# Kernel optimization log

Measured on AMD Instinct MI355X. Metric: run time of the kernel, lower is better.

The kernel has to match this reference:

```python
import jax, jax.numpy as jnp
import numpy as np

DT = 0.01
HID = 64
IN_DIM = 13  # obs_dim(6) + dynamic state(7)
G_VEC = jnp.array([0.0, 0.0, 9.81], dtype=jnp.float32)
MAG_REF = jnp.array([20.0, 0.0, -40.0], dtype=jnp.float32)


def q_multiply(q1, q2):
    w1, x1, y1, z1 = q1[:, 0], q1[:, 1], q1[:, 2], q1[:, 3]
    w2, x2, y2, z2 = q2[:, 0], q2[:, 1], q2[:, 2], q2[:, 3]
    w = w1 * w2 - x1 * x2 - y1 * y2 - z1 * z2
    x = w1 * x2 + x1 * w2 + y1 * z2 - z1 * y2
    y = w1 * y2 - x1 * z2 + y1 * w2 + z1 * x2
    z = w1 * z2 + x1 * y2 - y1 * x2 + z1 * w2
    return jnp.stack((w, x, y, z), axis=1)


def q_to_rot(q):
    w, x, y, z = q[:, 0], q[:, 1], q[:, 2], q[:, 3]
    r00 = 1 - 2 * (y * y + z * z); r01 = 2 * (x * y - z * w); r02 = 2 * (x * z + y * w)
    r10 = 2 * (x * y + z * w); r11 = 1 - 2 * (x * x + z * z); r12 = 2 * (y * z - x * w)
    r20 = 2 * (x * z - y * w); r21 = 2 * (y * z + x * w); r22 = 1 - 2 * (x * x + y * y)
    row0 = jnp.stack((r00, r01, r02), axis=1)
    row1 = jnp.stack((r10, r11, r12), axis=1)
    row2 = jnp.stack((r20, r21, r22), axis=1)
    return jnp.stack((row0, row1, row2), axis=1)  # [B,3,3]


def rotate_vec(q, v):
    return jnp.einsum('bij,bj->bi', q_to_rot(q), v)


def rotate_vec_inverse(q, v):
    return jnp.einsum('bji,bj->bi', q_to_rot(q), v)  # R^T v


def layer_norm(x, gamma, beta, eps=1e-5):
    mu = jnp.mean(x, axis=-1, keepdims=True)
    var = jnp.mean((x - mu) ** 2, axis=-1, keepdims=True)
    return (x - mu) * jax.lax.rsqrt(var + eps) * gamma + beta


def gru_cell(x, h, w_ih, w_hh, b_ih, b_hh):
    gi = x @ w_ih.T + b_ih  # [B, 3H]
    gh = h @ w_hh.T + b_hh
    i_r, i_z, i_n = jnp.split(gi, 3, axis=-1)
    h_r, h_z, h_n = jnp.split(gh, 3, axis=-1)
    r = jax.nn.sigmoid(i_r + h_r)
    z = jax.nn.sigmoid(i_z + h_z)
    n = jnp.tanh(i_n + r * h_n)
    return (1.0 - z) * n + z * h


def kalmannet_forward(inputs, ln_gamma, ln_beta, w_ih, w_hh, b_ih, b_hh, fc_w, fc_b):
    B, T, _ = inputs.shape
    x0 = jnp.zeros((B, 10), dtype=inputs.dtype).at[:, 6].set(1.0)
    h0 = jnp.zeros((B, HID), dtype=inputs.dtype)
    g_b = jnp.broadcast_to(G_VEC, (B, 3))
    mag_b = jnp.broadcast_to(MAG_REF, (B, 3))

    def step(carry, inp_t):
        x_curr, h_gru = carry
        accel = inp_t[:, 0:3]; gyro = inp_t[:, 3:6]; mag = inp_t[:, 6:9]
        p, v, q = x_curr[:, 0:3], x_curr[:, 3:6], x_curr[:, 6:10]
        # quaternion propagation
        half_ang = gyro * (DT * 0.5)
        dq = jnp.concatenate((jnp.ones((B, 1), inp_t.dtype), half_ang), axis=1)
        dq = dq / jnp.linalg.norm(dq, axis=1, keepdims=True)
        q_pred = q_multiply(q, dq)
        q_pred = q_pred / jnp.linalg.norm(q_pred, axis=1, keepdims=True)
        # strapdown kinematics
        accel_world = rotate_vec(q, accel) - g_b
        v_pred = v + accel_world * DT
        p_pred = p + v * DT + 0.5 * accel_world * (DT * DT)
        x_pred_pv = jnp.concatenate((p_pred, v_pred), axis=1)
        # innovation
        g_body = rotate_vec_inverse(q_pred, g_b)
        mag_body = rotate_vec_inverse(q_pred, mag_b)
        innovation = jnp.concatenate((mag, accel), axis=1) - jnp.concatenate((mag_body, g_body), axis=1)
        # learned Kalman gain
        gru_in = jnp.concatenate((innovation, v_pred, q_pred), axis=1)  # [B,13]
        gru_in = layer_norm(gru_in, ln_gamma, ln_beta)
        h_new = gru_cell(gru_in, h_gru, w_ih, w_hh, b_ih, b_hh)
        K = (h_new @ fc_w.T + fc_b).reshape(B, 6, 6)
        corr = jnp.einsum('bij,bj->bi', K, innovation)
        x_new = jnp.concatenate((x_pred_pv + corr, q_pred), axis=1)
        return (x_new, h_new), x_new

    inputs_t = jnp.swapaxes(inputs, 0, 1)  # [T,B,9]
    _, outs = jax.lax.scan(step, (x0, h0), inputs_t)
    return jnp.swapaxes(outs, 0, 1)  # [B,T,10]


def setup_inputs() -> dict:
    key = jax.random.key(0)
    ks = jax.random.split(key, 4)
    B, T = 4096, 512
    inputs = jax.random.normal(ks[0], (B, T, 9), dtype=jnp.float32)
    w_ih = jax.random.normal(ks[1], (3 * HID, IN_DIM), dtype=jnp.float32) * 0.1
    w_hh = jax.random.normal(ks[2], (3 * HID, HID), dtype=jnp.float32) * 0.1
    fc_w = jax.random.uniform(ks[3], (36, HID), minval=-0.001, maxval=0.001, dtype=jnp.float32)
    return {
        'inputs': inputs,
        'ln_gamma': jnp.ones((IN_DIM,), jnp.float32),
        'ln_beta': jnp.zeros((IN_DIM,), jnp.float32),
        'w_ih': w_ih,
        'w_hh': w_hh,
        'b_ih': jnp.zeros((3 * HID,), jnp.float32),
        'b_hh': jnp.zeros((3 * HID,), jnp.float32),
        'fc_w': fc_w,
        'fc_b': jnp.zeros((36,), jnp.float32),
    }


def reference(inputs, ln_gamma, ln_beta, w_ih, w_hh, b_ih, b_hh, fc_w, fc_b):
    return kalmannet_forward(inputs, ln_gamma, ln_beta, w_ih, w_hh, b_ih, b_hh, fc_w, fc_b)
```

## Files before the change

### kernel.cpp

```cpp
#include <hip/hip_runtime.h>

#define TT 512

typedef _Float16 h2_t  __attribute__((ext_vector_type(2)));
typedef _Float16 f16x4 __attribute__((ext_vector_type(4)));
typedef float    f32x4 __attribute__((ext_vector_type(4)));
typedef float    f32x4u __attribute__((ext_vector_type(4), aligned(4)));
typedef unsigned int u32x2_t __attribute__((ext_vector_type(2)));

__device__ __forceinline__ float frcp(float x){ return __builtin_amdgcn_rcpf(x); }
__device__ __forceinline__ float frsq(float x){ return __builtin_amdgcn_rsqf(x); }
__device__ __forceinline__ float sigm(float x){ return frcp(1.0f + __expf(-x)); }
__device__ __forceinline__ float tanh_fast(float x){
    x = fminf(15.0f, fmaxf(-15.0f, x));
    float e = __expf(2.0f * x);
    return (e - 1.0f) * frcp(e + 1.0f);
}
__device__ __forceinline__ float fdot2(h2_t a, h2_t b, float c){
    return __builtin_amdgcn_fdot2(a, b, c, false);
}
__device__ __forceinline__ h2_t pk16(float a, float b){
    return __builtin_bit_cast(h2_t, __builtin_amdgcn_cvt_pkrtz(a, b));
}
__device__ __forceinline__ f16x4 mk4(float a, float b, float c, float d){
    u32x2_t u;
    u[0] = __builtin_bit_cast(unsigned int, pk16(a, b));
    u[1] = __builtin_bit_cast(unsigned int, pk16(c, d));
    return __builtin_bit_cast(f16x4, u);
}
__device__ __forceinline__ f32x4 mfma16(f16x4 a, f16x4 b, f32x4 c){
    return __builtin_amdgcn_mfma_f32_16x16x16f16(a, b, c, 0, 0, 0);
}

__global__
__attribute__((amdgpu_flat_work_group_size(256, 256), amdgpu_waves_per_eu(1, 1)))
void kalman_kernel(const float* __restrict__ inputs,
                   const float* __restrict__ ln_gamma,
                   const float* __restrict__ ln_beta,
                   const float* __restrict__ w_ih,
                   const float* __restrict__ w_hh,
                   const float* __restrict__ b_ih,
                   const float* __restrict__ b_hh,
                   const float* __restrict__ fc_w,
                   const float* __restrict__ fc_b,
                   float* __restrict__ out)
{
    __shared__ u32x2_t     s_h[4][64];
    __shared__ unsigned int s_Kp[24][16];

    const int tid  = threadIdx.x;
    const int lane = tid & 63;
    const int w    = tid >> 6;
    const int bq   = lane & 15;
    const int g    = lane >> 4;
    const int e    = blockIdx.x * 16 + bq;

    const int mtR = w, mtZ = 4 + w, mtN = 8 + w;

    f16x4 whhR[4], whhZ[4], whhN[4];
#pragma unroll
    for (int kt = 0; kt < 4; ++kt) {
        const float* rR = w_hh + (size_t)(16 * mtR + bq) * 64 + 16 * kt + 4 * g;
        const float* rZ = w_hh + (size_t)(16 * mtZ + bq) * 64 + 16 * kt + 4 * g;
        const float* rN = w_hh + (size_t)(16 * mtN + bq) * 64 + 16 * kt + 4 * g;
        whhR[kt] = mk4(rR[0], rR[1], rR[2], rR[3]);
        whhZ[kt] = mk4(rZ[0], rZ[1], rZ[2], rZ[3]);
        whhN[kt] = mk4(rN[0], rN[1], rN[2], rN[3]);
    }

    f16x4 wihR, wihZ, wihN;
    {
        const float* rR = w_ih + (size_t)(16 * mtR + bq) * 13;
        const float* rZ = w_ih + (size_t)(16 * mtZ + bq) * 13;
        const float* rN = w_ih + (size_t)(16 * mtN + bq) * 13;
        const int k0 = 4 * g;
        const float m1 = (k0 + 1 < 13) ? 1.f : 0.f;
        const float m2 = (k0 + 2 < 13) ? 1.f : 0.f;
        const float m3 = (k0 + 3 < 13) ? 1.f : 0.f;
        wihR = mk4(rR[k0], m1 * rR[k0 + 1], m2 * rR[k0 + 2], m3 * rR[k0 + 3]);
        wihZ = mk4(rZ[k0], m1 * rZ[k0 + 1], m2 * rZ[k0 + 2], m3 * rZ[k0 + 3]);
        wihN = mk4(rN[k0], m1 * rN[k0 + 1], m2 * rN[k0 + 2], m3 * rN[k0 + 3]);
    }

    f16x4 fcA[4];
    {
        const int o = 16 * w + bq;
        const float* rp = fc_w + (size_t)(o < 36 ? o : 0) * 64;
        const float msk = (o < 36) ? 1.f : 0.f;
#pragma unroll
        for (int kt = 0; kt < 4; ++kt) {
            const float* cp = rp + 16 * kt + 4 * g;
            fcA[kt] = mk4(msk * cp[0], msk * cp[1], msk * cp[2], msk * cp[3]);
        }
    }

    f32x4 br, bz, bin, bhn, fcb4;
#pragma unroll
    for (int r = 0; r < 4; ++r) {
        const int oR = 16 * mtR + 4 * g + r;
        const int oZ = 16 * mtZ + 4 * g + r;
        const int oN = 16 * mtN + 4 * g + r;
        br[r]  = b_ih[oR] + b_hh[oR];
        bz[r]  = b_ih[oZ] + b_hh[oZ];
        bin[r] = b_ih[oN];
        bhn[r] = b_hh[oN];
        const int oF = 16 * w + 4 * g + r;
        fcb4[r] = (oF < 36) ? fc_b[oF] : 0.f;
    }

    float gamx[4], betx[4];
#pragma unroll
    for (int j = 0; j < 4; ++j) {
        const int k = 4 * g + j;
        gamx[j] = (k < 13) ? ln_gamma[k] : 0.f;
        betx[j] = (k < 13) ? ln_beta[k]  : 0.f;
    }

    float pos0 = 0, pos1 = 0, pos2 = 0, vel0 = 0, vel1 = 0, vel2 = 0;
    float q0 = 1.0f, q1 = 0, q2 = 0, q3 = 0;
    f32x4 hstate = f32x4{0.f, 0.f, 0.f, 0.f};
    f16x4 hB[4];
#pragma unroll
    for (int i = 0; i < 4; ++i) hB[i] = mk4(0.f, 0.f, 0.f, 0.f);

    const float* ip = inputs + (size_t)e * TT * 9;
    float*       op = out    + (size_t)e * TT * 10;

    float cur[9];
#pragma unroll
    for (int k = 0; k < 9; ++k) cur[k] = ip[k];

    for (int t = 0; t < TT; ++t) {
        f32x4 ar = br, az4 = bz, nhh = bhn;
#pragma unroll
        for (int kt = 0; kt < 4; ++kt) {
            ar  = mfma16(whhR[kt], hB[kt], ar);
            az4 = mfma16(whhZ[kt], hB[kt], az4);
            nhh = mfma16(whhN[kt], hB[kt], nhh);
        }

        const int tn = (t < TT - 1) ? (t + 1) : t;
        float nxt[9];
#pragma unroll
        for (int k = 0; k < 9; ++k) nxt[k] = ip[(size_t)tn * 9 + k];

        const float ax = cur[0], ay = cur[1], az = cur[2];
        const float gx = cur[3], gy = cur[4], gz = cur[5];
        const float mx = cur[6], my = cur[7], mz = cur[8];

        const float hx = gx * 0.005f, hy = gy * 0.005f, hz = gz * 0.005f;
        const float dn = frsq(1.0f + hx * hx + hy * hy + hz * hz);
        const float dw = dn, dx = hx * dn, dy = hy * dn, dz = hz * dn;
        float qpw = q0 * dw - q1 * dx - q2 * dy - q3 * dz;
        float qpx = q0 * dx + q1 * dw + q2 * dz - q3 * dy;
        float qpy = q0 * dy - q1 * dz + q2 * dw + q3 * dx;
        float qpz = q0 * dz + q1 * dy - q2 * dx + q3 * dw;
        const float pn = frsq(qpw * qpw + qpx * qpx + qpy * qpy + qpz * qpz);
        qpw *= pn; qpx *= pn; qpy *= pn; qpz *= pn;

        const float r00 = 1.0f - 2.0f * (q2 * q2 + q3 * q3);
        const float r01 = 2.0f * (q1 * q2 - q3 * q0);
        const float r02 = 2.0f * (q1 * q3 + q2 * q0);
        const float r10 = 2.0f * (q1 * q2 + q3 * q0);
        const float r11 = 1.0f - 2.0f * (q1 * q1 + q3 * q3);
        const float r12 = 2.0f * (q2 * q3 - q1 * q0);
        const float r20 = 2.0f * (q1 * q3 - q2 * q0);
        const float r21 = 2.0f * (q2 * q3 + q1 * q0);
        const float r22 = 1.0f - 2.0f * (q1 * q1 + q2 * q2);
        const float awx = r00 * ax + r01 * ay + r02 * az;
        const float awy = r10 * ax + r11 * ay + r12 * az;
        const float awz = r20 * ax + r21 * ay + r22 * az - 9.81f;

        const float vpx = vel0 + awx * 0.01f;
        const float vpy = vel1 + awy * 0.01f;
        const float vpz = vel2 + awz * 0.01f;
        const float ppx = pos0 + vel0 * 0.01f + awx * 5e-5f;
        const float ppy = pos1 + vel1 * 0.01f + awy * 5e-5f;
        const float ppz = pos2 + vel2 * 0.01f + awz * 5e-5f;

        const float s00 = 1.0f - 2.0f * (qpy * qpy + qpz * qpz);
        const float s01 = 2.0f * (qpx * qpy - qpz * qpw);
        const float s02 = 2.0f * (qpx * qpz + qpy * qpw);
        const float s20 = 2.0f * (qpx * qpz - qpy * qpw);
        const float s21 = 2.0f * (qpy * qpz + qpx * qpw);
        const float s22 = 1.0f - 2.0f * (qpx * qpx + qpy * qpy);
        const float gbx = 9.81f * s20, gby = 9.81f * s21, gbz = 9.81f * s22;
        const float mbx = 20.0f * s00 - 40.0f * s20;
        const float mby = 20.0f * s01 - 40.0f * s21;
        const float mbz = 20.0f * s02 - 40.0f * s22;

        float inn[6];
        inn[0] = mx - mbx; inn[1] = my - mby; inn[2] = mz - mbz;
        inn[3] = ax - gbx; inn[4] = ay - gby; inn[5] = az - gbz;

        float gin[13];
        gin[0] = inn[0]; gin[1] = inn[1]; gin[2] = inn[2];
        gin[3] = inn[3]; gin[4] = inn[4]; gin[5] = inn[5];
        gin[6] = vpx; gin[7] = vpy; gin[8] = vpz;
        gin[9] = qpw; gin[10] = qpx; gin[11] = qpy; gin[12] = qpz;

        float mu = 0.0f;
#pragma unroll
        for (int k = 0; k < 13; ++k) mu += gin[k];
        mu *= (1.0f / 13.0f);
        float var = 0.0f;
#pragma unroll
        for (int k = 0; k < 13; ++k) { const float d = gin[k] - mu; var += d * d; }
        var *= (1.0f / 13.0f);
        const float sc = frsq(var + 1e-5f);

        const float xs0 = g == 0 ? gin[0] : g == 1 ? gin[4] : g == 2 ? gin[8]  : gin[12];
        const float xs1 = g == 0 ? gin[1] : g == 1 ? gin[5] : g == 2 ? gin[9]  : 0.f;
        const float xs2 = g == 0 ? gin[2] : g == 1 ? gin[6] : g == 2 ? gin[10] : 0.f;
        const float xs3 = g == 0 ? gin[3] : g == 1 ? gin[7] : g == 2 ? gin[11] : 0.f;
        const f16x4 xB = mk4((xs0 - mu) * sc * gamx[0] + betx[0],
                             (xs1 - mu) * sc * gamx[1] + betx[1],
                             (xs2 - mu) * sc * gamx[2] + betx[2],
                             (xs3 - mu) * sc * gamx[3] + betx[3]);

        ar  = mfma16(wihR, xB, ar);
        az4 = mfma16(wihZ, xB, az4);
        const f32x4 nin = mfma16(wihN, xB, bin);

        f32x4 hv = hstate;
#pragma unroll
        for (int r = 0; r < 4; ++r) {
            const float rr = sigm(ar[r]);
            const float zz = sigm(az4[r]);
            const float nn = tanh_fast(nin[r] + rr * nhh[r]);
            hv[r] = fmaf(zz, hv[r] - nn, nn);
        }
        hstate = hv;
        const f16x4 hOwn = mk4(hv[0], hv[1], hv[2], hv[3]);

        s_h[w][lane] = __builtin_bit_cast(u32x2_t, hOwn);
        __syncthreads();
#pragma unroll
        for (int kt = 0; kt < 4; ++kt)
            hB[kt] = __builtin_bit_cast(f16x4, s_h[kt][lane]);

        if (w < 3) {
            f32x4 a = mfma16(fcA[0], hB[0], fcb4);
#pragma unroll
            for (int kt = 1; kt < 4; ++kt) a = mfma16(fcA[kt], hB[kt], a);
            s_Kp[8 * w + 2 * g][bq]     = __builtin_bit_cast(unsigned int, pk16(a[0], a[1]));
            s_Kp[8 * w + 2 * g + 1][bq] = __builtin_bit_cast(unsigned int, pk16(a[2], a[3]));
        }
        __syncthreads();

        h2_t K2[18];
#pragma unroll
        for (int rp = 0; rp < 18; ++rp)
            K2[rp] = __builtin_bit_cast(h2_t, s_Kp[rp][bq]);

        const h2_t inn2_0 = pk16(inn[0], inn[1]);
        const h2_t inn2_1 = pk16(inn[2], inn[3]);
        const h2_t inn2_2 = pk16(inn[4], inn[5]);
        float c[6];
#pragma unroll
        for (int i = 0; i < 6; ++i)
            c[i] = fdot2(K2[3 * i + 0], inn2_0,
                   fdot2(K2[3 * i + 1], inn2_1,
                   fdot2(K2[3 * i + 2], inn2_2, 0.f)));

        pos0 = ppx + c[0]; pos1 = ppy + c[1]; pos2 = ppz + c[2];
        vel0 = vpx + c[3]; vel1 = vpy + c[4]; vel2 = vpz + c[5];
        q0 = qpw; q1 = qpx; q2 = qpy; q3 = qpz;

        if (w == 0) {
            float* o0 = op + (size_t)t * 10;
            if (g == 0) {
                *(f32x4u*)(o0) = f32x4u{pos0, pos1, pos2, vel0};
            } else if (g == 1) {
                *(f32x4u*)(o0 + 4) = f32x4u{vel1, vel2, q0, q1};
            } else if (g == 2) {
                o0[8] = q2; o0[9] = q3;
            }
        }

#pragma unroll
        for (int k = 0; k < 9; ++k) cur[k] = nxt[k];
    }
}

extern "C" void kernel_launch(void* const* d_in, const int* in_sizes, int n_in,
                              void* d_out, int out_size, void* d_ws, size_t ws_size,
                              hipStream_t stream) {
    const float* inputs   = (const float*)d_in[0];
    const float* ln_gamma = (const float*)d_in[1];
    const float* ln_beta  = (const float*)d_in[2];
    const float* w_ih     = (const float*)d_in[3];
    const float* w_hh     = (const float*)d_in[4];
    const float* b_ih     = (const float*)d_in[5];
    const float* b_hh     = (const float*)d_in[6];
    const float* fc_w     = (const float*)d_in[7];
    const float* fc_b     = (const float*)d_in[8];
    float* out = (float*)d_out;

    const int B = in_sizes[0] / (TT * 9);
    kalman_kernel<<<dim3(B / 16), dim3(256), 0, stream>>>(
        inputs, ln_gamma, ln_beta, w_ih, w_hh, b_ih, b_hh, fc_w, fc_b, out);
}
```

Baseline: 700.9 us.

## Software-pipeline recurrence: precompute next-step quaternion/innovation work between barriers

Splits each timestep into a HEAD part that depends only on the quaternion and inputs (quaternion propagation, rotation, innovations, partial layer-norm sums) and an ASTEP part needing the Kalman-corrected position and velocity. HEAD for step t+1 now runs while the FC gain MFMA for step t executes, before the barrier, so it leaves the serial critical path. Layer-norm statistics are rebuilt from precomputed partial sums and variance is computed as E[x^2]-mu^2. Inputs are prefetched two steps ahead with vector loads. The single-pass variance can be less accurate, and the restructured loop makes register pressure and control flow more complex.

New measurement: 786.1 us. 1.12x slower.

```diff
diff --git a/kernel.cpp b/kernel.cpp
--- a/kernel.cpp
+++ b/kernel.cpp
@@ -116,8 +116,13 @@
         betx[j] = (k < 13) ? ln_beta[k]  : 0.f;
     }
 
-    float pos0 = 0, pos1 = 0, pos2 = 0, vel0 = 0, vel1 = 0, vel2 = 0;
-    float q0 = 1.0f, q1 = 0, q2 = 0, q3 = 0;
+    float q0 = 1.0f, q1 = 0.f, q2 = 0.f, q3 = 0.f;
+    float qpn0, qpn1, qpn2, qpn3;
+    float aw0, aw1, aw2;
+    float innc0, innc1, innc2, innc3, innc4, innc5;
+    float innx0, innx1, innx2, innx3, innx4, innx5;
+    float S1h, S2h;
+    float vpx, vpy, vpz, ppx, ppy, ppz;
     f32x4 hstate = f32x4{0.f, 0.f, 0.f, 0.f};
     f16x4 hB[4];
 #pragma unroll
@@ -126,37 +131,23 @@
     const float* ip = inputs + (size_t)e * TT * 9;
     float*       op = out    + (size_t)e * TT * 10;
 
-    float cur[9];
+    float cur[9], nxt[9];
 #pragma unroll
     for (int k = 0; k < 9; ++k) cur[k] = ip[k];
 
-    for (int t = 0; t < TT; ++t) {
-        f32x4 ar = br, az4 = bz, nhh = bhn;
-#pragma unroll
-        for (int kt = 0; kt < 4; ++kt) {
-            ar  = mfma16(whhR[kt], hB[kt], ar);
-            az4 = mfma16(whhZ[kt], hB[kt], az4);
-            nhh = mfma16(whhN[kt], hB[kt], nhh);
-        }
-
-        const int tn = (t < TT - 1) ? (t + 1) : t;
-        float nxt[9];
-#pragma unroll
-        for (int k = 0; k < 9; ++k) nxt[k] = ip[(size_t)tn * 9 + k];
-
+    auto HEAD = [&]() {
         const float ax = cur[0], ay = cur[1], az = cur[2];
         const float gx = cur[3], gy = cur[4], gz = cur[5];
         const float mx = cur[6], my = cur[7], mz = cur[8];
-
         const float hx = gx * 0.005f, hy = gy * 0.005f, hz = gz * 0.005f;
         const float dn = frsq(1.0f + hx * hx + hy * hy + hz * hz);
         const float dw = dn, dx = hx * dn, dy = hy * dn, dz = hz * dn;
-        float qpw = q0 * dw - q1 * dx - q2 * dy - q3 * dz;
-        float qpx = q0 * dx + q1 * dw + q2 * dz - q3 * dy;
-        float qpy = q0 * dy - q1 * dz + q2 * dw + q3 * dx;
-        float qpz = q0 * dz + q1 * dy - q2 * dx + q3 * dw;
-        const float pn = frsq(qpw * qpw + qpx * qpx + qpy * qpy + qpz * qpz);
-        qpw *= pn; qpx *= pn; qpy *= pn; qpz *= pn;
+        const float a0 = q0 * dw - q1 * dx - q2 * dy - q3 * dz;
+        const float a1 = q0 * dx + q1 * dw + q2 * dz - q3 * dy;
+        const float a2 = q0 * dy - q1 * dz + q2 * dw + q3 * dx;
+        const float a3 = q0 * dz + q1 * dy - q2 * dx + q3 * dw;
+        const float pn = frsq(a0 * a0 + a1 * a1 + a2 * a2 + a3 * a3);
+        qpn0 = a0 * pn; qpn1 = a1 * pn; qpn2 = a2 * pn; qpn3 = a3 * pn;
 
         const float r00 = 1.0f - 2.0f * (q2 * q2 + q3 * q3);
         const float r01 = 2.0f * (q1 * q2 - q3 * q0);
@@ -167,56 +158,65 @@
         const float r20 = 2.0f * (q1 * q3 - q2 * q0);
         const float r21 = 2.0f * (q2 * q3 + q1 * q0);
         const float r22 = 1.0f - 2.0f * (q1 * q1 + q2 * q2);
-        const float awx = r00 * ax + r01 * ay + r02 * az;
-        const float awy = r10 * ax + r11 * ay + r12 * az;
-        const float awz = r20 * ax + r21 * ay + r22 * az - 9.81f;
-
-        const float vpx = vel0 + awx * 0.01f;
-        const float vpy = vel1 + awy * 0.01f;
-        const float vpz = vel2 + awz * 0.01f;
-        const float ppx = pos0 + vel0 * 0.01f + awx * 5e-5f;
-        const float ppy = pos1 + vel1 * 0.01f + awy * 5e-5f;
-        const float ppz = pos2 + vel2 * 0.01f + awz * 5e-5f;
-
-        const float s00 = 1.0f - 2.0f * (qpy * qpy + qpz * qpz);
-        const float s01 = 2.0f * (qpx * qpy - qpz * qpw);
-        const float s02 = 2.0f * (qpx * qpz + qpy * qpw);
-        const float s20 = 2.0f * (qpx * qpz - qpy * qpw);
-        const float s21 = 2.0f * (qpy * qpz + qpx * qpw);
-        const float s22 = 1.0f - 2.0f * (qpx * qpx + qpy * qpy);
-        const float gbx = 9.81f * s20, gby = 9.81f * s21, gbz = 9.81f * s22;
-        const float mbx = 20.0f * s00 - 40.0f * s20;
-        const float mby = 20.0f * s01 - 40.0f * s21;
-        const float mbz = 20.0f * s02 - 40.0f * s22;
-
-        float inn[6];
-        inn[0] = mx - mbx; inn[1] = my - mby; inn[2] = mz - mbz;
-        inn[3] = ax - gbx; inn[4] = ay - gby; inn[5] = az - gbz;
-
-        float gin[13];
-        gin[0] = inn[0]; gin[1] = inn[1]; gin[2] = inn[2];
-        gin[3] = inn[3]; gin[4] = inn[4]; gin[5] = inn[5];
-        gin[6] = vpx; gin[7] = vpy; gin[8] = vpz;
-        gin[9] = qpw; gin[10] = qpx; gin[11] = qpy; gin[12] = qpz;
-
-        float mu = 0.0f;
-#pragma unroll
-        for (int k = 0; k < 13; ++k) mu += gin[k];
-        mu *= (1.0f / 13.0f);
-        float var = 0.0f;
-#pragma unroll
-        for (int k = 0; k < 13; ++k) { const float d = gin[k] - mu; var += d * d; }
-        var *= (1.0f / 13.0f);
+        aw0 = r00 * ax + r01 * ay + r02 * az;
+        aw1 = r10 * ax + r11 * ay + r12 * az;
+        aw2 = r20 * ax + r21 * ay + r22 * az - 9.81f;
+
+        const float s00 = 1.0f - 2.0f * (qpn2 * qpn2 + qpn3 * qpn3);
+        const float s01 = 2.0f * (qpn1 * qpn2 - qpn3 * qpn0);
+        const float s02 = 2.0f * (qpn1 * qpn3 + qpn2 * qpn0);
+        const float s20 = 2.0f * (qpn1 * qpn3 - qpn2 * qpn0);
+        const float s21 = 2.0f * (qpn2 * qpn3 + qpn1 * qpn0);
+        const float s22 = 1.0f - 2.0f * (qpn1 * qpn1 + qpn2 * qpn2);
+        innx0 = mx - (20.0f * s00 - 40.0f * s20);
+        innx1 = my - (20.0f * s01 - 40.0f * s21);
+        innx2 = mz - (20.0f * s02 - 40.0f * s22);
+        innx3 = ax - 9.81f * s20;
+        innx4 = ay - 9.81f * s21;
+        innx5 = az - 9.81f * s22;
+
+        S1h = ((innx0 + innx1) + (innx2 + innx3)) + ((innx4 + innx5) +
+              (qpn0 + qpn1)) + (qpn2 + qpn3);
+        float s2 = innx0 * innx0;
+        s2 = fmaf(innx1, innx1, s2); s2 = fmaf(innx2, innx2, s2);
+        s2 = fmaf(innx3, innx3, s2); s2 = fmaf(innx4, innx4, s2);
+        s2 = fmaf(innx5, innx5, s2); s2 = fmaf(qpn0, qpn0, s2);
+        s2 = fmaf(qpn1, qpn1, s2);   s2 = fmaf(qpn2, qpn2, s2);
+        s2 = fmaf(qpn3, qpn3, s2);
+        S2h = s2;
+    };
+
+    auto ASTEP = [&](float pn0, float pn1, float pn2,
+                     float vn0, float vn1, float vn2) {
+        f32x4 ar = br, az4 = bz, nhh = bhn;
+#pragma unroll
+        for (int kt = 0; kt < 4; ++kt) {
+            ar  = mfma16(whhR[kt], hB[kt], ar);
+            az4 = mfma16(whhZ[kt], hB[kt], az4);
+            nhh = mfma16(whhN[kt], hB[kt], nhh);
+        }
+
+        vpx = fmaf(aw0, 0.01f, vn0);
+        vpy = fmaf(aw1, 0.01f, vn1);
+        vpz = fmaf(aw2, 0.01f, vn2);
+        ppx = fmaf(vn0, 0.01f, fmaf(aw0, 5e-5f, pn0));
+        ppy = fmaf(vn1, 0.01f, fmaf(aw1, 5e-5f, pn1));
+        ppz = fmaf(vn2, 0.01f, fmaf(aw2, 5e-5f, pn2));
+
+        const float mu = (S1h + ((vpx + vpy) + vpz)) * (1.0f / 13.0f);
+        float s2 = S2h;
+        s2 = fmaf(vpx, vpx, s2); s2 = fmaf(vpy, vpy, s2); s2 = fmaf(vpz, vpz, s2);
+        const float var = fmaf(-mu, mu, s2 * (1.0f / 13.0f));
         const float sc = frsq(var + 1e-5f);
 
-        const float xs0 = g == 0 ? gin[0] : g == 1 ? gin[4] : g == 2 ? gin[8]  : gin[12];
-        const float xs1 = g == 0 ? gin[1] : g == 1 ? gin[5] : g == 2 ? gin[9]  : 0.f;
-        const float xs2 = g == 0 ? gin[2] : g == 1 ? gin[6] : g == 2 ? gin[10] : 0.f;
-        const float xs3 = g == 0 ? gin[3] : g == 1 ? gin[7] : g == 2 ? gin[11] : 0.f;
-        const f16x4 xB = mk4((xs0 - mu) * sc * gamx[0] + betx[0],
-                             (xs1 - mu) * sc * gamx[1] + betx[1],
-                             (xs2 - mu) * sc * gamx[2] + betx[2],
-                             (xs3 - mu) * sc * gamx[3] + betx[3]);
+        const float c0 = g == 0 ? innx0 : g == 1 ? innx4 : g == 2 ? vpz  : qpn3;
+        const float c1 = g == 0 ? innx1 : g == 1 ? innx5 : g == 2 ? qpn0 : 0.f;
+        const float c2 = g == 0 ? innx2 : g == 1 ? vpx   : g == 2 ? qpn1 : 0.f;
+        const float c3 = g == 0 ? innx3 : g == 1 ? vpy   : g == 2 ? qpn2 : 0.f;
+        const f16x4 xB = mk4((c0 - mu) * sc * gamx[0] + betx[0],
+                             (c1 - mu) * sc * gamx[1] + betx[1],
+                             (c2 - mu) * sc * gamx[2] + betx[2],
+                             (c3 - mu) * sc * gamx[3] + betx[3]);
 
         ar  = mfma16(wihR, xB, ar);
         az4 = mfma16(wihZ, xB, az4);
@@ -232,12 +232,33 @@
         }
         hstate = hv;
         const f16x4 hOwn = mk4(hv[0], hv[1], hv[2], hv[3]);
-
         s_h[w][lane] = __builtin_bit_cast(u32x2_t, hOwn);
-        __syncthreads();
+
+        innc0 = innx0; innc1 = innx1; innc2 = innx2;
+        innc3 = innx3; innc4 = innx4; innc5 = innx5;
+        q0 = qpn0; q1 = qpn1; q2 = qpn2; q3 = qpn3;
+    };
+
+    HEAD();
+    ASTEP(0.f, 0.f, 0.f, 0.f, 0.f, 0.f);
+#pragma unroll
+    for (int k = 0; k < 9; ++k) cur[k] = ip[9 + k];
+    __syncthreads();
+
+    for (int t = 0; t < TT; ++t) {
 #pragma unroll
         for (int kt = 0; kt < 4; ++kt)
             hB[kt] = __builtin_bit_cast(f16x4, s_h[kt][lane]);
+
+        {
+            const int tf = (t + 2 < TT) ? (t + 2) : (TT - 1);
+            const float* np = ip + (size_t)tf * 9;
+            const f32x4u v0 = *(const f32x4u*)np;
+            const f32x4u v1 = *(const f32x4u*)(np + 4);
+            nxt[0] = v0[0]; nxt[1] = v0[1]; nxt[2] = v0[2]; nxt[3] = v0[3];
+            nxt[4] = v1[0]; nxt[5] = v1[1]; nxt[6] = v1[2]; nxt[7] = v1[3];
+            nxt[8] = np[8];
+        }
 
         if (w < 3) {
             f32x4 a = mfma16(fcA[0], hB[0], fcb4);
@@ -246,6 +267,8 @@
             s_Kp[8 * w + 2 * g][bq]     = __builtin_bit_cast(unsigned int, pk16(a[0], a[1]));
             s_Kp[8 * w + 2 * g + 1][bq] = __builtin_bit_cast(unsigned int, pk16(a[2], a[3]));
         }
+
+        if (t < TT - 1) HEAD();
         __syncthreads();
 
         h2_t K2[18];
@@ -253,33 +276,36 @@
         for (int rp = 0; rp < 18; ++rp)
             K2[rp] = __builtin_bit_cast(h2_t, s_Kp[rp][bq]);
 
-        const h2_t inn2_0 = pk16(inn[0], inn[1]);
-        const h2_t inn2_1 = pk16(inn[2], inn[3]);
-        const h2_t inn2_2 = pk16(inn[4], inn[5]);
+        const h2_t in0 = pk16(innc0, innc1);
+        const h2_t in1 = pk16(innc2, innc3);
+        const h2_t in2 = pk16(innc4, innc5);
         float c[6];
 #pragma unroll
         for (int i = 0; i < 6; ++i)
-            c[i] = fdot2(K2[3 * i + 0], inn2_0,
-                   fdot2(K2[3 * i + 1], inn2_1,
-                   fdot2(K2[3 * i + 2], inn2_2, 0.f)));
-
-        pos0 = ppx + c[0]; pos1 = ppy + c[1]; pos2 = ppz + c[2];
-        vel0 = vpx + c[3]; vel1 = vpy + c[4]; vel2 = vpz + c[5];
-        q0 = qpw; q1 = qpx; q2 = qpy; q3 = qpz;
+            c[i] = fdot2(K2[3 * i + 0], in0,
+                   fdot2(K2[3 * i + 1], in1,
+                   fdot2(K2[3 * i + 2], in2, 0.f)));
+
+        const float pn0 = ppx + c[0], pn1 = ppy + c[1], pn2 = ppz + c[2];
+        const float vn0 = vpx + c[3], vn1 = vpy + c[4], vn2 = vpz + c[5];
 
         if (w == 0) {
             float* o0 = op + (size_t)t * 10;
             if (g == 0) {
-                *(f32x4u*)(o0) = f32x4u{pos0, pos1, pos2, vel0};
+                *(f32x4u*)(o0) = f32x4u{pn0, pn1, pn2, vn0};
             } else if (g == 1) {
-                *(f32x4u*)(o0 + 4) = f32x4u{vel1, vel2, q0, q1};
+                *(f32x4u*)(o0 + 4) = f32x4u{vn1, vn2, q0, q1};
             } else if (g == 2) {
                 o0[8] = q2; o0[9] = q3;
             }
         }
 
+        if (t == TT - 1) break;
+
+        ASTEP(pn0, pn1, pn2, vn0, vn1, vn2);
 #pragma unroll
         for (int k = 0; k < 9; ++k) cur[k] = nxt[k];
+        __syncthreads();
     }
 }
 
```

## Compute fc gain redundantly per wave and double-buffer hidden state to drop barrier

Applied to the files above, without the earlier changes.

Each wave now computes all three fc output tiles itself, 12 MFMAs instead of 4, and redistributes the packed gain values within the wave using ds_bpermute instead of sharing them through LDS. This removes the second __syncthreads per timestep. The hidden-state LDS buffer is double-buffered so the single remaining barrier is enough to avoid write-after-read hazards. The cost is extra MFMA work and more registers for the replicated fc weights on a serial, latency-bound recurrence.

Result: slower. 899.3 us (+28.3%).

```diff
diff --git a/kernel.cpp b/kernel.cpp
--- a/kernel.cpp
+++ b/kernel.cpp
@@ -45,8 +45,7 @@
                    const float* __restrict__ fc_b,
                    float* __restrict__ out)
 {
-    __shared__ u32x2_t     s_h[4][64];
-    __shared__ unsigned int s_Kp[24][16];
+    __shared__ u32x2_t s_h[2][4][64];
 
     const int tid  = threadIdx.x;
     const int lane = tid & 63;
@@ -82,19 +81,20 @@
         wihN = mk4(rN[k0], m1 * rN[k0 + 1], m2 * rN[k0 + 2], m3 * rN[k0 + 3]);
     }
 
-    f16x4 fcA[4];
-    {
-        const int o = 16 * w + bq;
+    f16x4 fcA[3][4];
+#pragma unroll
+    for (int mt = 0; mt < 3; ++mt) {
+        const int o = 16 * mt + bq;
         const float* rp = fc_w + (size_t)(o < 36 ? o : 0) * 64;
         const float msk = (o < 36) ? 1.f : 0.f;
 #pragma unroll
         for (int kt = 0; kt < 4; ++kt) {
             const float* cp = rp + 16 * kt + 4 * g;
-            fcA[kt] = mk4(msk * cp[0], msk * cp[1], msk * cp[2], msk * cp[3]);
-        }
-    }
-
-    f32x4 br, bz, bin, bhn, fcb4;
+            fcA[mt][kt] = mk4(msk * cp[0], msk * cp[1], msk * cp[2], msk * cp[3]);
+        }
+    }
+
+    f32x4 br, bz, bin, bhn;
 #pragma unroll
     for (int r = 0; r < 4; ++r) {
         const int oR = 16 * mtR + 4 * g + r;
@@ -104,9 +104,15 @@
         bz[r]  = b_ih[oZ] + b_hh[oZ];
         bin[r] = b_ih[oN];
         bhn[r] = b_hh[oN];
-        const int oF = 16 * w + 4 * g + r;
-        fcb4[r] = (oF < 36) ? fc_b[oF] : 0.f;
-    }
+    }
+    f32x4 fcb4[3];
+#pragma unroll
+    for (int mt = 0; mt < 3; ++mt)
+#pragma unroll
+        for (int r = 0; r < 4; ++r) {
+            const int o = 16 * mt + 4 * g + r;
+            fcb4[mt][r] = (o < 36) ? fc_b[o] : 0.f;
+        }
 
     float gamx[4], betx[4];
 #pragma unroll
@@ -116,6 +122,10 @@
         betx[j] = (k < 13) ? ln_beta[k]  : 0.f;
     }
 
+    int paddr[4];
+#pragma unroll
+    for (int gp = 0; gp < 4; ++gp) paddr[gp] = (bq + 16 * gp) << 2;
+
     float pos0 = 0, pos1 = 0, pos2 = 0, vel0 = 0, vel1 = 0, vel2 = 0;
     float q0 = 1.0f, q1 = 0, q2 = 0, q3 = 0;
     f32x4 hstate = f32x4{0.f, 0.f, 0.f, 0.f};
@@ -129,6 +139,8 @@
     float cur[9];
 #pragma unroll
     for (int k = 0; k < 9; ++k) cur[k] = ip[k];
+
+    int p = 0;
 
     for (int t = 0; t < TT; ++t) {
         f32x4 ar = br, az4 = bz, nhh = bhn;
@@ -233,25 +245,32 @@
         hstate = hv;
         const f16x4 hOwn = mk4(hv[0], hv[1], hv[2], hv[3]);
 
-        s_h[w][lane] = __builtin_bit_cast(u32x2_t, hOwn);
+        s_h[p][w][lane] = __builtin_bit_cast(u32x2_t, hOwn);
         __syncthreads();
 #pragma unroll
         for (int kt = 0; kt < 4; ++kt)
-            hB[kt] = __builtin_bit_cast(f16x4, s_h[kt][lane]);
-
-        if (w < 3) {
-            f32x4 a = mfma16(fcA[0], hB[0], fcb4);
-#pragma unroll
-            for (int kt = 1; kt < 4; ++kt) a = mfma16(fcA[kt], hB[kt], a);
-            s_Kp[8 * w + 2 * g][bq]     = __builtin_bit_cast(unsigned int, pk16(a[0], a[1]));
-            s_Kp[8 * w + 2 * g + 1][bq] = __builtin_bit_cast(unsigned int, pk16(a[2], a[3]));
-        }
-        __syncthreads();
+            hB[kt] = __builtin_bit_cast(f16x4, s_h[p][kt][lane]);
+
+        int kp[3][2];
+#pragma unroll
+        for (int mt = 0; mt < 3; ++mt) {
+            f32x4 a = mfma16(fcA[mt][0], hB[0], fcb4[mt]);
+#pragma unroll
+            for (int kt = 1; kt < 4; ++kt) a = mfma16(fcA[mt][kt], hB[kt], a);
+            kp[mt][0] = __builtin_bit_cast(int, pk16(a[0], a[1]));
+            kp[mt][1] = __builtin_bit_cast(int, pk16(a[2], a[3]));
+        }
 
         h2_t K2[18];
 #pragma unroll
-        for (int rp = 0; rp < 18; ++rp)
-            K2[rp] = __builtin_bit_cast(h2_t, s_Kp[rp][bq]);
+        for (int mt = 0; mt < 2; ++mt)
+#pragma unroll
+            for (int gp = 0; gp < 4; ++gp) {
+                K2[8 * mt + 2 * gp + 0] = __builtin_bit_cast(h2_t, __builtin_amdgcn_ds_bpermute(paddr[gp], kp[mt][0]));
+                K2[8 * mt + 2 * gp + 1] = __builtin_bit_cast(h2_t, __builtin_amdgcn_ds_bpermute(paddr[gp], kp[mt][1]));
+            }
+        K2[16] = __builtin_bit_cast(h2_t, __builtin_amdgcn_ds_bpermute(paddr[0], kp[2][0]));
+        K2[17] = __builtin_bit_cast(h2_t, __builtin_amdgcn_ds_bpermute(paddr[0], kp[2][1]));
 
         const h2_t inn2_0 = pk16(inn[0], inn[1]);
         const h2_t inn2_1 = pk16(inn[2], inn[3]);
@@ -278,6 +297,7 @@
             }
         }
 
+        p ^= 1;
 #pragma unroll
         for (int k = 0; k < 9; ++k) cur[k] = nxt[k];
     }
```
